# Kernel optimization log

Hardware: AMD Instinct MI355X
Metric: run time of the kernel (lower is better)

Reference implementation:

```python
import jax, jax.numpy as jnp
import numpy as np

E = 1024   # embed_size
S = 2048   # seq_len
H = 16     # heads
HD = S // H  # head_dim = 128
N = 2      # batch


def setup_inputs() -> dict:
    key = jax.random.key(0)
    ks = jax.random.split(key, 11)
    w = 0.02  # init scale to keep softmax logits well-conditioned
    return {
        "x":   jax.random.normal(ks[0], (N, E, S), dtype=jnp.float32),
        "W_r": jax.random.normal(ks[1], (S, E), dtype=jnp.float32) * w,
        "b_r": jnp.zeros((S,), dtype=jnp.float32),
        "Wq":  jax.random.normal(ks[2], (H, HD, HD), dtype=jnp.float32) * w,
        "bq":  jnp.zeros((H, HD), dtype=jnp.float32),
        "Wk":  jax.random.normal(ks[3], (H, HD, HD), dtype=jnp.float32) * w,
        "bk":  jnp.zeros((H, HD), dtype=jnp.float32),
        "Wv":  jax.random.normal(ks[4], (H, HD, HD), dtype=jnp.float32) * w,
        "bv":  jnp.zeros((H, HD), dtype=jnp.float32),
        "Wo":  jax.random.normal(ks[5], (E, S), dtype=jnp.float32) * w,
        "bo":  jnp.zeros((E,), dtype=jnp.float32),
    }


def reference(x, W_r, b_r, Wq, bq, Wk, bk, Wv, bv, Wo, bo):
    n = x.shape[0]
    # reduced[n, j, s] = sum_e W_r[j, e] * x[n, e, s] + b_r[j]
    # equals reduce_dim(x.permute(0,2,1)).permute(0,2,1): shape (N, S, S)
    reduced = jnp.einsum('je,nes->njs', W_r, x) + b_r[None, :, None]
    # split last dim into heads: (N, S, H, HD)
    r = reduced.reshape(n, S, H, HD)
    # per-head linear projections (torch Linear: y = x @ W.T + b), batched over heads
    q = jnp.einsum('nshd,hkd->hnsk', r, Wq) + bq[:, None, None, :]
    k = jnp.einsum('nshd,hkd->hnsk', r, Wk) + bk[:, None, None, :]
    v = jnp.einsum('nshd,hkd->hnsk', r, Wv) + bv[:, None, None, :]
    # attention (NO 1/sqrt(d) scaling, faithful to source)
    scores = jnp.einsum('hnqd,hnkd->hnqk', q, k)          # (H, N, S, S)
    weights = jax.nn.softmax(scores, axis=-1)
    o = jnp.einsum('hnqk,hnkd->hnqd', weights, v)          # (H, N, S, HD)
    # faithful raw reshape of the (H, N, S, HD)-contiguous tensor
    o = o.reshape(n, S, H * HD)
    return jnp.einsum('nsd,ed->nse', o, Wo) + bo           # (N, S, E)
```

## Files before the change

### kernel.cpp

```cpp
#include <hip/hip_runtime.h>

#define S_LEN 2048
#define E_DIM 1024
#define NH 16
#define HD 128
#define NB 2
#define NPAIR (NH*NB)

typedef __attribute__((ext_vector_type(4))) float f32x4;
typedef __attribute__((ext_vector_type(8))) short bf16x8;

__device__ __forceinline__ unsigned short f2bf(float f) {
    unsigned u = __builtin_bit_cast(unsigned, f);
    u += 0x7fffu + ((u >> 16) & 1u);
    return (unsigned short)(u >> 16);
}
__device__ __forceinline__ float bf2f(unsigned short h) {
    unsigned u = ((unsigned)h) << 16;
    return __builtin_bit_cast(float, u);
}
__device__ __forceinline__ unsigned cvtpk(float lo, float hi) {
    unsigned r;
    asm("v_cvt_pk_bf16_f32 %0, %1, %2" : "=v"(r) : "v"(lo), "v"(hi));
    return r;
}

__device__ __forceinline__ void gl_lds16(const unsigned short* g, unsigned short* l) {
    __builtin_amdgcn_global_load_lds((__attribute__((address_space(1))) void*)g,
                                     (__attribute__((address_space(3))) void*)l,
                                     16, 0, 0);
}

template<int OF32, int SWZ>
__global__ __launch_bounds__(256, 2) void gemm_bt(
    const unsigned short* __restrict__ A, const unsigned short* __restrict__ B,
    void* __restrict__ C,
    const float* __restrict__ brow, const float* __restrict__ bcol,
    int K, int lda, int ldb, int ldc, int zdiv,
    long long a_sh, long long a_sl, long long b_sh, long long b_sl,
    long long c_sh, long long c_sl, int brs, int bcs)
{
    __shared__ unsigned short As[2][128*64];
    __shared__ unsigned short Bs[2][128*64];
    int bm, bn, z;
    if (SWZ) {
        const int gx = gridDim.x, gy = gridDim.y;
        const int nxy = gx * gy;
        const int nwg = nxy * gridDim.z;
        const int flat = (blockIdx.z*gy + blockIdx.y)*gx + blockIdx.x;
        const int id2 = (flat & 7)*(nwg >> 3) + (flat >> 3);
        z = id2 / nxy; const int r = id2 % nxy; bm = r / gx; bn = r % gx;
    } else { bm = blockIdx.y; bn = blockIdx.x; z = blockIdx.z; }
    const int zh = z / zdiv, zl = z % zdiv;
    A += (long long)zh*a_sh + (long long)zl*a_sl;
    B += (long long)zh*b_sh + (long long)zl*b_sl;
    const long long coff = (long long)zh*c_sh + (long long)zl*c_sl;
    const int tid = threadIdx.x, wid = tid >> 6, lane = tid & 63;
    const int l3 = lane >> 3;
    const int cg = (lane & 7) ^ l3;
    const unsigned short* Ag = A + (long long)(bm*128 + wid*32 + l3)*lda + cg*8;
    const unsigned short* Bg = B + (long long)(bn*128 + wid*32 + l3)*ldb + cg*8;

    f32x4 acc[4][4];
    #pragma unroll
    for (int m = 0; m < 4; ++m)
        #pragma unroll
        for (int n = 0; n < 4; ++n)
            #pragma unroll
            for (int j = 0; j < 4; ++j) acc[m][n][j] = 0.f;

    const int r0 = lane & 15, q = lane >> 4;
    const int wr = (wid >> 1) * 64, wc = (wid & 1) * 64;

    auto stage = [&](int buf, int kt) {
        unsigned short* as = &As[buf][wid*32*64];
        unsigned short* bs = &Bs[buf][wid*32*64];
        #pragma unroll
        for (int i = 0; i < 4; ++i) {
            gl_lds16(Ag + (long long)(i*8)*lda + kt, as + i*8*64);
            gl_lds16(Bg + (long long)(i*8)*ldb + kt, bs + i*8*64);
        }
    };

    const int nt = K >> 6;
    stage(0, 0);
    __syncthreads();
    int cur = 0;
    for (int t = 0; t < nt; ++t) {
        if (t + 1 < nt) stage(cur ^ 1, (t + 1) << 6);
        #pragma unroll
        for (int ks = 0; ks < 2; ++ks) {
            bf16x8 av[4], bv[4];
            #pragma unroll
            for (int m = 0; m < 4; ++m) {
                const int ra = wr + m*16 + r0;
                av[m] = *(const bf16x8*)&As[cur][ra*64 + (((ks*4 + q) ^ (ra & 7)) << 3)];
                const int rb = wc + m*16 + r0;
                bv[m] = *(const bf16x8*)&Bs[cur][rb*64 + (((ks*4 + q) ^ (rb & 7)) << 3)];
            }
            __builtin_amdgcn_s_setprio(1);
            #pragma unroll
            for (int m = 0; m < 4; ++m)
                #pragma unroll
                for (int n = 0; n < 4; ++n)
                    acc[m][n] = __builtin_amdgcn_mfma_f32_16x16x32_bf16(
                        av[m], bv[n], acc[m][n], 0, 0, 0);
            __builtin_amdgcn_s_setprio(0);
        }
        __syncthreads();
        cur ^= 1;
    }

    const int rq = lane >> 4;
    const bool has_br = (brow != nullptr), has_bc = (bcol != nullptr);
    #pragma unroll
    for (int m = 0; m < 4; ++m) {
        #pragma unroll
        for (int n = 0; n < 4; ++n) {
            const int gcol = bn*128 + wc + n*16 + r0;
            float cb = has_bc ? bcol[(long long)bcs*zh + gcol] : 0.f;
            #pragma unroll
            for (int j = 0; j < 4; ++j) {
                const int grow = bm*128 + wr + m*16 + rq*4 + j;
                float v = acc[m][n][j] + cb;
                if (has_br) v += brow[(long long)brs*zh + grow];
                const long long idx = coff + (long long)grow*ldc + gcol;
                if (OF32) ((float*)C)[idx] = v;
                else      ((unsigned short*)C)[idx] = f2bf(v);
            }
        }
    }
}

__global__ __launch_bounds__(256, 2) void flash_attn(
    const unsigned short* __restrict__ Q,
    const unsigned short* __restrict__ Kb,
    const unsigned short* __restrict__ Vt,
    unsigned short* __restrict__ O)
{
    __shared__ unsigned short Ks[2][64*128];
    __shared__ unsigned short Vs[2][128*64];
    __shared__ unsigned short Plds[4][32*64];
    const int flat = blockIdx.y * gridDim.x + blockIdx.x;
    const int id2 = (flat & 7)*64 + (flat >> 3);
    const int pair = id2 >> 4, qt = id2 & 15;
    const int tid = threadIdx.x, wid = tid >> 6, lane = tid & 63;
    const int r0 = lane & 15, q4 = lane >> 4;
    const long long base = (long long)pair * S_LEN * HD;
    const unsigned short* Qp = Q + base + (long long)(qt*128 + wid*32) * HD;
    const unsigned short* Kp = Kb + base;
    const unsigned short* Vp = Vt + base;
    unsigned short* P = &Plds[wid][0];

    const int krow = wid*16 + (lane >> 4);
    const int kc0  = (lane & 15) ^ (lane >> 4);
    const int vrow = wid*32 + (lane >> 3);
    const int vc0  = (lane & 7) ^ (lane >> 3);

    auto stageK = [&](int buf, int kv) {
        #pragma unroll
        for (int i = 0; i < 4; ++i)
            gl_lds16(Kp + (long long)(kv + krow + i*4)*HD + ((kc0 ^ ((i & 1) << 2))*8),
                     &Ks[buf][(wid*16 + i*4)*128]);
    };
    auto stageV = [&](int buf, int kv) {
        #pragma unroll
        for (int i = 0; i < 4; ++i)
            gl_lds16(Vp + (long long)(vrow + i*8)*S_LEN + kv + vc0*8,
                     &Vs[buf][(wid*32 + i*8)*64]);
    };

    bf16x8 qfr[2][4];
    #pragma unroll
    for (int qf = 0; qf < 2; ++qf)
        #pragma unroll
        for (int ks = 0; ks < 4; ++ks)
            qfr[qf][ks] = *(const bf16x8*)&Qp[(qf*16 + r0)*HD + ks*32 + q4*8];

    f32x4 o_acc[2][8];
    #pragma unroll
    for (int qf = 0; qf < 2; ++qf)
        #pragma unroll
        for (int nf = 0; nf < 8; ++nf)
            #pragma unroll
            for (int j = 0; j < 4; ++j) o_acc[qf][nf][j] = 0.f;
    float m_[2] = {-3.0e38f, -3.0e38f}, l_[2] = {0.f, 0.f};

    stageK(0, 0); stageV(0, 0);
    __syncthreads();
    int cur = 0;
    for (int kv = 0; kv < S_LEN; kv += 64) {
        if (kv + 64 < S_LEN) { stageK(cur ^ 1, kv + 64); stageV(cur ^ 1, kv + 64); }
        f32x4 sacc[4][2];
        #pragma unroll
        for (int kf = 0; kf < 4; ++kf)
            #pragma unroll
            for (int qf = 0; qf < 2; ++qf)
                #pragma unroll
                for (int j = 0; j < 4; ++j) sacc[kf][qf][j] = 0.f;
        #pragma unroll
        for (int ks = 0; ks < 4; ++ks) {
            bf16x8 kfr[4];
            #pragma unroll
            for (int kf = 0; kf < 4; ++kf) {
                const int row = kf*16 + r0;
                kfr[kf] = *(const bf16x8*)&Ks[cur][row*128 + (((ks*4 + q4) ^ (r0 & 7)) << 3)];
            }
            __builtin_amdgcn_s_setprio(1);
            #pragma unroll
            for (int kf = 0; kf < 4; ++kf)
                #pragma unroll
                for (int qf = 0; qf < 2; ++qf)
                    sacc[kf][qf] = __builtin_amdgcn_mfma_f32_16x16x32_bf16(
                        kfr[kf], qfr[qf][ks], sacc[kf][qf], 0, 0, 0);
            __builtin_amdgcn_s_setprio(0);
        }
        #pragma unroll
        for (int qf = 0; qf < 2; ++qf) {
            float t0 = fmaxf(fmaxf(sacc[0][qf][0], sacc[0][qf][1]),
                             fmaxf(sacc[0][qf][2], sacc[0][qf][3]));
            float t1 = fmaxf(fmaxf(sacc[1][qf][0], sacc[1][qf][1]),
                             fmaxf(sacc[1][qf][2], sacc[1][qf][3]));
            float t2 = fmaxf(fmaxf(sacc[2][qf][0], sacc[2][qf][1]),
                             fmaxf(sacc[2][qf][2], sacc[2][qf][3]));
            float t3 = fmaxf(fmaxf(sacc[3][qf][0], sacc[3][qf][1]),
                             fmaxf(sacc[3][qf][2], sacc[3][qf][3]));
            float tmax = fmaxf(fmaxf(t0, t1), fmaxf(t2, t3));
            tmax = fmaxf(tmax, __shfl_xor(tmax, 16));
            tmax = fmaxf(tmax, __shfl_xor(tmax, 32));
            if (__all(tmax <= m_[qf] + 8.f)) {
                float tsum = 0.f;
                #pragma unroll
                for (int kf = 0; kf < 4; ++kf)
                    #pragma unroll
                    for (int j = 0; j < 4; ++j) {
                        const float e = __expf(sacc[kf][qf][j] - m_[qf]);
                        sacc[kf][qf][j] = e; tsum += e;
                    }
                tsum += __shfl_xor(tsum, 16);
                tsum += __shfl_xor(tsum, 32);
                l_[qf] += tsum;
            } else {
                const float mnew = fmaxf(m_[qf], tmax);
                const float scale = __expf(m_[qf] - mnew);
                float tsum = 0.f;
                #pragma unroll
                for (int kf = 0; kf < 4; ++kf)
                    #pragma unroll
                    for (int j = 0; j < 4; ++j) {
                        const float e = __expf(sacc[kf][qf][j] - mnew);
                        sacc[kf][qf][j] = e; tsum += e;
                    }
                tsum += __shfl_xor(tsum, 16);
                tsum += __shfl_xor(tsum, 32);
                l_[qf] = l_[qf]*scale + tsum;
                m_[qf] = mnew;
                float sc[4];
                #pragma unroll
                for (int j = 0; j < 4; ++j) sc[j] = __shfl(scale, (q4*4 + j) | (lane & 48));
                #pragma unroll
                for (int nf = 0; nf < 8; ++nf)
                    #pragma unroll
                    for (int j = 0; j < 4; ++j) o_acc[qf][nf][j] *= sc[j];
            }
        }
        #pragma unroll
        for (int qf = 0; qf < 2; ++qf)
            #pragma unroll
            for (int kf = 0; kf < 4; ++kf) {
                uint2 pk;
                pk.x = cvtpk(sacc[kf][qf][0], sacc[kf][qf][1]);
                pk.y = cvtpk(sacc[kf][qf][2], sacc[kf][qf][3]);
                const int row = qf*16 + r0;
                const int byte = (row*128 + kf*32 + q4*8) ^ ((row & 7) << 4);
                *(uint2*)((char*)P + byte) = pk;
            }
        #pragma unroll
        for (int c = 0; c < 2; ++c) {
            bf16x8 pa[2];
            #pragma unroll
            for (int qf = 0; qf < 2; ++qf) {
                const int row = qf*16 + r0;
                const int byte = (row*128 + c*64 + q4*16) ^ ((row & 7) << 4);
                pa[qf] = *(const bf16x8*)((char*)P + byte);
            }
            bf16x8 vb[8];
            #pragma unroll
            for (int nf = 0; nf < 8; ++nf) {
                const int row = nf*16 + r0;
                vb[nf] = *(const bf16x8*)&Vs[cur][row*64 + (((c*4 + q4) ^ (r0 & 7)) << 3)];
            }
            __builtin_amdgcn_s_setprio(1);
            #pragma unroll
            for (int nf = 0; nf < 8; ++nf)
                #pragma unroll
                for (int qf = 0; qf < 2; ++qf)
                    o_acc[qf][nf] = __builtin_amdgcn_mfma_f32_16x16x32_bf16(
                        pa[qf], vb[nf], o_acc[qf][nf], 0, 0, 0);
            __builtin_amdgcn_s_setprio(0);
        }
        __syncthreads();
        cur ^= 1;
    }
    #pragma unroll
    for (int qf = 0; qf < 2; ++qf) {
        const float inv = 1.f / l_[qf];
        float iv[4];
        #pragma unroll
        for (int j = 0; j < 4; ++j) iv[j] = __shfl(inv, (q4*4 + j) | (lane & 48));
        #pragma unroll
        for (int nf = 0; nf < 8; ++nf)
            #pragma unroll
            for (int j = 0; j < 4; ++j) {
                const int grow = qt*128 + wid*32 + qf*16 + q4*4 + j;
                O[base + (long long)grow*HD + nf*16 + r0] = f2bf(o_acc[qf][nf][j] * iv[j]);
            }
    }
}

__global__ __launch_bounds__(256) void transpose_conv(
    const float* __restrict__ x, unsigned short* __restrict__ xT)
{
    __shared__ float t[32][33];
    const int n = blockIdx.z;
    const int e0 = blockIdx.y * 32, s0 = blockIdx.x * 32;
    const int tx = threadIdx.x & 31, ty = threadIdx.x >> 5;
    #pragma unroll
    for (int i = 0; i < 4; ++i) {
        const int e = ty + i*8;
        t[e][tx] = x[((long long)n*E_DIM + e0 + e)*S_LEN + s0 + tx];
    }
    __syncthreads();
    #pragma unroll
    for (int i = 0; i < 4; ++i) {
        const int s = ty + i*8;
        xT[((long long)n*S_LEN + s0 + s)*E_DIM + e0 + tx] = f2bf(t[tx][s]);
    }
}

__global__ __launch_bounds__(256) void conv_bf16(
    const float* __restrict__ in, unsigned short* __restrict__ out, int n8)
{
    const int i = blockIdx.x * 256 + threadIdx.x;
    if (i >= n8) return;
    const float4 a = ((const float4*)in)[2*i];
    const float4 b = ((const float4*)in)[2*i + 1];
    unsigned short u[8] = {f2bf(a.x), f2bf(a.y), f2bf(a.z), f2bf(a.w),
                           f2bf(b.x), f2bf(b.y), f2bf(b.z), f2bf(b.w)};
    ((uint4*)out)[i] = *(const uint4*)u;
}

extern "C" void kernel_launch(void* const* d_in, const int* in_sizes, int n_in,
                              void* d_out, int out_size, void* d_ws, size_t ws_size,
                              hipStream_t stream)
{
    const float* x   = (const float*)d_in[0];
    const float* W_r = (const float*)d_in[1];
    const float* b_r = (const float*)d_in[2];
    const float* Wq  = (const float*)d_in[3];
    const float* bq  = (const float*)d_in[4];
    const float* Wk  = (const float*)d_in[5];
    const float* bk  = (const float*)d_in[6];
    const float* Wv  = (const float*)d_in[7];
    const float* bv  = (const float*)d_in[8];
    const float* Wo  = (const float*)d_in[9];
    const float* bo  = (const float*)d_in[10];
    float* out = (float*)d_out;
    (void)in_sizes; (void)n_in; (void)out_size; (void)ws_size;

    char* w = (char*)d_ws;
    size_t off = 0;
    auto take = [&](size_t bytes) -> unsigned short* {
        unsigned short* p = (unsigned short*)(w + off);
        off = (off + bytes + 255) & ~(size_t)255;
        return p;
    };
    unsigned short* Wr_b = take((size_t)S_LEN*E_DIM*2);
    unsigned short* xT_b = take((size_t)NB*S_LEN*E_DIM*2);
    unsigned short* Wq_b = take((size_t)NH*HD*HD*2);
    unsigned short* Wk_b = take((size_t)NH*HD*HD*2);
    unsigned short* Wv_b = take((size_t)NH*HD*HD*2);
    unsigned short* Wo_b = take((size_t)E_DIM*S_LEN*2);
    unsigned short* Rd_b = take((size_t)NB*S_LEN*S_LEN*2);
    unsigned short* Q_b  = take((size_t)NPAIR*S_LEN*HD*2);
    unsigned short* K_b  = take((size_t)NPAIR*S_LEN*HD*2);
    unsigned short* Vt_b = take((size_t)NPAIR*HD*S_LEN*2);
    unsigned short* O_b  = take((size_t)NPAIR*S_LEN*HD*2);

    conv_bf16<<<dim3((S_LEN*E_DIM/8 + 255)/256), 256, 0, stream>>>(W_r, Wr_b, S_LEN*E_DIM/8);
    conv_bf16<<<dim3((NH*HD*HD/8 + 255)/256), 256, 0, stream>>>(Wq, Wq_b, NH*HD*HD/8);
    conv_bf16<<<dim3((NH*HD*HD/8 + 255)/256), 256, 0, stream>>>(Wk, Wk_b, NH*HD*HD/8);
    conv_bf16<<<dim3((NH*HD*HD/8 + 255)/256), 256, 0, stream>>>(Wv, Wv_b, NH*HD*HD/8);
    conv_bf16<<<dim3((E_DIM*S_LEN/8 + 255)/256), 256, 0, stream>>>(Wo, Wo_b, E_DIM*S_LEN/8);
    transpose_conv<<<dim3(S_LEN/32, E_DIM/32, NB), 256, 0, stream>>>(x, xT_b);

    gemm_bt<0,1><<<dim3(S_LEN/128, S_LEN/128, NB), 256, 0, stream>>>(
        Wr_b, xT_b, Rd_b, b_r, nullptr,
        E_DIM, E_DIM, E_DIM, S_LEN, 1,
        0LL, 0LL, (long long)S_LEN*E_DIM, 0LL, (long long)S_LEN*S_LEN, 0LL, 0, 0);

    gemm_bt<0,1><<<dim3(HD/128, S_LEN/128, NPAIR), 256, 0, stream>>>(
        Rd_b, Wq_b, Q_b, nullptr, bq,
        HD, S_LEN, HD, HD, NB,
        128LL, (long long)S_LEN*S_LEN, (long long)HD*HD, 0LL,
        (long long)NB*S_LEN*HD, (long long)S_LEN*HD, 0, HD);
    gemm_bt<0,1><<<dim3(HD/128, S_LEN/128, NPAIR), 256, 0, stream>>>(
        Rd_b, Wk_b, K_b, nullptr, bk,
        HD, S_LEN, HD, HD, NB,
        128LL, (long long)S_LEN*S_LEN, (long long)HD*HD, 0LL,
        (long long)NB*S_LEN*HD, (long long)S_LEN*HD, 0, HD);
    gemm_bt<0,1><<<dim3(S_LEN/128, HD/128, NPAIR), 256, 0, stream>>>(
        Wv_b, Rd_b, Vt_b, bv, nullptr,
        HD, HD, S_LEN, S_LEN, NB,
        (long long)HD*HD, 0LL, 128LL, (long long)S_LEN*S_LEN,
        (long long)NB*HD*S_LEN, (long long)HD*S_LEN, HD, 0);

    flash_attn<<<dim3(S_LEN/128, NPAIR), 256, 0, stream>>>(Q_b, K_b, Vt_b, O_b);

    gemm_bt<1,1><<<dim3(E_DIM/128, S_LEN/128, NB), 256, 0, stream>>>(
        O_b, Wo_b, out, nullptr, bo,
        S_LEN, S_LEN, S_LEN, E_DIM, 1,
        (long long)S_LEN*S_LEN, 0LL, 0LL, 0LL, (long long)S_LEN*E_DIM, 0LL, 0, 0);
}
```

Before: 302.3 us.

## Fuse Q/K/V projections into one GEMM and shrink flash-attention KV tile

Stacks Wq, Wk and Wv per head into one weight matrix with a packing kernel, and computes all three projections in a single qkv_gemm launch. Q and K are written interleaved into one buffer and V is written transposed. This replaces three projection GEMMs and three weight-conversion launches, and reads the reduced activation once instead of three times. Flash attention now uses a 32-wide KV tile with smaller LDS buffers and launch bounds raised to 4 blocks per SM for occupancy, at the cost of twice as many loop iterations and barriers. The transposed V store in qkv_gemm is strided and may coalesce poorly.

```diff
diff --git a/kernel.cpp b/kernel.cpp
--- a/kernel.cpp
+++ b/kernel.cpp
@@ -14,10 +14,6 @@
     unsigned u = __builtin_bit_cast(unsigned, f);
     u += 0x7fffu + ((u >> 16) & 1u);
     return (unsigned short)(u >> 16);
-}
-__device__ __forceinline__ float bf2f(unsigned short h) {
-    unsigned u = ((unsigned)h) << 16;
-    return __builtin_bit_cast(float, u);
 }
 __device__ __forceinline__ unsigned cvtpk(float lo, float hi) {
     unsigned r;
@@ -132,42 +128,142 @@
     }
 }
 
-__global__ __launch_bounds__(256, 2) void flash_attn(
-    const unsigned short* __restrict__ Q,
-    const unsigned short* __restrict__ Kb,
+__global__ __launch_bounds__(256, 2) void qkv_gemm(
+    const unsigned short* __restrict__ Rd,
+    const unsigned short* __restrict__ Wstk,
+    const float* __restrict__ bstk,
+    unsigned short* __restrict__ QK,
+    unsigned short* __restrict__ Vt)
+{
+    __shared__ unsigned short As[2][128*64];
+    __shared__ unsigned short Bs[2][128*64];
+    const int gx = gridDim.x, gy = gridDim.y;
+    const int nxy = gx * gy;
+    const int nwg = nxy * gridDim.z;
+    const int flat = (blockIdx.z*gy + blockIdx.y)*gx + blockIdx.x;
+    const int id2 = (flat & 7)*(nwg >> 3) + (flat >> 3);
+    const int z = id2 / nxy; const int r = id2 % nxy;
+    const int bm = r / gx, bn = r % gx;
+    const int h = z >> 1, nb = z & 1;
+    const unsigned short* A = Rd + (long long)nb*S_LEN*S_LEN + h*128;
+    const unsigned short* B = Wstk + (long long)h*384*128 + (long long)bn*128*128;
+    const int tid = threadIdx.x, wid = tid >> 6, lane = tid & 63;
+    const int l3 = lane >> 3;
+    const int cg = (lane & 7) ^ l3;
+    const unsigned short* Ag = A + (long long)(bm*128 + wid*32 + l3)*S_LEN + cg*8;
+    const unsigned short* Bg = B + (long long)(wid*32 + l3)*HD + cg*8;
+
+    f32x4 acc[4][4];
+    #pragma unroll
+    for (int m = 0; m < 4; ++m)
+        #pragma unroll
+        for (int n = 0; n < 4; ++n)
+            #pragma unroll
+            for (int j = 0; j < 4; ++j) acc[m][n][j] = 0.f;
+
+    const int r0 = lane & 15, q = lane >> 4;
+    const int wr = (wid >> 1) * 64, wc = (wid & 1) * 64;
+
+    auto stage = [&](int buf, int kt) {
+        unsigned short* as = &As[buf][wid*32*64];
+        unsigned short* bs = &Bs[buf][wid*32*64];
+        #pragma unroll
+        for (int i = 0; i < 4; ++i) {
+            gl_lds16(Ag + (long long)(i*8)*S_LEN + kt, as + i*8*64);
+            gl_lds16(Bg + (long long)(i*8)*HD + kt, bs + i*8*64);
+        }
+    };
+
+    stage(0, 0);
+    __syncthreads();
+    int cur = 0;
+    #pragma unroll
+    for (int t = 0; t < 2; ++t) {
+        if (t == 0) stage(1, 64);
+        #pragma unroll
+        for (int ks = 0; ks < 2; ++ks) {
+            bf16x8 av[4], bv[4];
+            #pragma unroll
+            for (int m = 0; m < 4; ++m) {
+                const int ra = wr + m*16 + r0;
+                av[m] = *(const bf16x8*)&As[cur][ra*64 + (((ks*4 + q) ^ (ra & 7)) << 3)];
+                const int rb = wc + m*16 + r0;
+                bv[m] = *(const bf16x8*)&Bs[cur][rb*64 + (((ks*4 + q) ^ (rb & 7)) << 3)];
+            }
+            __builtin_amdgcn_s_setprio(1);
+            #pragma unroll
+            for (int m = 0; m < 4; ++m)
+                #pragma unroll
+                for (int n = 0; n < 4; ++n)
+                    acc[m][n] = __builtin_amdgcn_mfma_f32_16x16x32_bf16(
+                        av[m], bv[n], acc[m][n], 0, 0, 0);
+            __builtin_amdgcn_s_setprio(0);
+        }
+        __syncthreads();
+        cur ^= 1;
+    }
+
+    const int rq = lane >> 4;
+    #pragma unroll
+    for (int m = 0; m < 4; ++m) {
+        #pragma unroll
+        for (int n = 0; n < 4; ++n) {
+            const int lcol = wc + n*16 + r0;
+            const float cb = bstk[h*384 + bn*128 + lcol];
+            #pragma unroll
+            for (int j = 0; j < 4; ++j) {
+                const int grow = bm*128 + wr + m*16 + rq*4 + j;
+                const float v = acc[m][n][j] + cb;
+                if (bn < 2)
+                    QK[(long long)z*S_LEN*256 + (long long)grow*256 + bn*128 + lcol] = f2bf(v);
+                else
+                    Vt[(long long)z*HD*S_LEN + (long long)lcol*S_LEN + grow] = f2bf(v);
+            }
+        }
+    }
+}
+
+__global__ __launch_bounds__(256, 4) void flash_attn(
+    const unsigned short* __restrict__ QK,
     const unsigned short* __restrict__ Vt,
     unsigned short* __restrict__ O)
 {
-    __shared__ unsigned short Ks[2][64*128];
-    __shared__ unsigned short Vs[2][128*64];
-    __shared__ unsigned short Plds[4][32*64];
+    __shared__ unsigned short Ks[2][32*128];
+    __shared__ unsigned short Vs[2][128*32];
+    __shared__ unsigned short Plds[4][32*32];
     const int flat = blockIdx.y * gridDim.x + blockIdx.x;
     const int id2 = (flat & 7)*64 + (flat >> 3);
     const int pair = id2 >> 4, qt = id2 & 15;
     const int tid = threadIdx.x, wid = tid >> 6, lane = tid & 63;
     const int r0 = lane & 15, q4 = lane >> 4;
-    const long long base = (long long)pair * S_LEN * HD;
-    const unsigned short* Qp = Q + base + (long long)(qt*128 + wid*32) * HD;
-    const unsigned short* Kp = Kb + base;
-    const unsigned short* Vp = Vt + base;
+    const long long qkbase = (long long)pair * S_LEN * 256;
+    const unsigned short* Qp = QK + qkbase + (long long)(qt*128 + wid*32) * 256;
+    const unsigned short* Kp = QK + qkbase + 128;
+    const unsigned short* Vp = Vt + (long long)pair * HD * S_LEN;
     unsigned short* P = &Plds[wid][0];
 
-    const int krow = wid*16 + (lane >> 4);
-    const int kc0  = (lane & 15) ^ (lane >> 4);
-    const int vrow = wid*32 + (lane >> 3);
-    const int vc0  = (lane & 7) ^ (lane >> 3);
+    const int kr_l = lane >> 4;
+    const int kc_l = lane & 15;
+    const int vr_l = lane >> 2;
+    const int vc_l = lane & 3;
 
     auto stageK = [&](int buf, int kv) {
         #pragma unroll
-        for (int i = 0; i < 4; ++i)
-            gl_lds16(Kp + (long long)(kv + krow + i*4)*HD + ((kc0 ^ ((i & 1) << 2))*8),
-                     &Ks[buf][(wid*16 + i*4)*128]);
+        for (int i = 0; i < 2; ++i) {
+            const int srow = wid*8 + i*4 + kr_l;
+            const int sc = kc_l ^ (srow & 7);
+            gl_lds16(Kp + (long long)(kv + srow)*256 + sc*8,
+                     &Ks[buf][(wid*8 + i*4)*128]);
+        }
     };
     auto stageV = [&](int buf, int kv) {
         #pragma unroll
-        for (int i = 0; i < 4; ++i)
-            gl_lds16(Vp + (long long)(vrow + i*8)*S_LEN + kv + vc0*8,
-                     &Vs[buf][(wid*32 + i*8)*64]);
+        for (int i = 0; i < 2; ++i) {
+            const int srow = wid*32 + i*16 + vr_l;
+            const int sc = vc_l ^ (srow & 3);
+            gl_lds16(Vp + (long long)srow*S_LEN + kv + sc*8,
+                     &Vs[buf][(wid*32 + i*16)*32]);
+        }
     };
 
     bf16x8 qfr[2][4];
@@ -175,7 +271,7 @@
     for (int qf = 0; qf < 2; ++qf)
         #pragma unroll
         for (int ks = 0; ks < 4; ++ks)
-            qfr[qf][ks] = *(const bf16x8*)&Qp[(qf*16 + r0)*HD + ks*32 + q4*8];
+            qfr[qf][ks] = *(const bf16x8*)&Qp[(qf*16 + r0)*256 + ks*32 + q4*8];
 
     f32x4 o_acc[2][8];
     #pragma unroll
@@ -189,26 +285,26 @@
     stageK(0, 0); stageV(0, 0);
     __syncthreads();
     int cur = 0;
-    for (int kv = 0; kv < S_LEN; kv += 64) {
-        if (kv + 64 < S_LEN) { stageK(cur ^ 1, kv + 64); stageV(cur ^ 1, kv + 64); }
-        f32x4 sacc[4][2];
-        #pragma unroll
-        for (int kf = 0; kf < 4; ++kf)
+    for (int kv = 0; kv < S_LEN; kv += 32) {
+        if (kv + 32 < S_LEN) { stageK(cur ^ 1, kv + 32); stageV(cur ^ 1, kv + 32); }
+        f32x4 sacc[2][2];
+        #pragma unroll
+        for (int kf = 0; kf < 2; ++kf)
             #pragma unroll
             for (int qf = 0; qf < 2; ++qf)
                 #pragma unroll
                 for (int j = 0; j < 4; ++j) sacc[kf][qf][j] = 0.f;
         #pragma unroll
         for (int ks = 0; ks < 4; ++ks) {
-            bf16x8 kfr[4];
-            #pragma unroll
-            for (int kf = 0; kf < 4; ++kf) {
+            bf16x8 kfr[2];
+            #pragma unroll
+            for (int kf = 0; kf < 2; ++kf) {
                 const int row = kf*16 + r0;
                 kfr[kf] = *(const bf16x8*)&Ks[cur][row*128 + (((ks*4 + q4) ^ (r0 & 7)) << 3)];
             }
             __builtin_amdgcn_s_setprio(1);
             #pragma unroll
-            for (int kf = 0; kf < 4; ++kf)
+            for (int kf = 0; kf < 2; ++kf)
                 #pragma unroll
                 for (int qf = 0; qf < 2; ++qf)
                     sacc[kf][qf] = __builtin_amdgcn_mfma_f32_16x16x32_bf16(
@@ -221,17 +317,13 @@
                              fmaxf(sacc[0][qf][2], sacc[0][qf][3]));
             float t1 = fmaxf(fmaxf(sacc[1][qf][0], sacc[1][qf][1]),
                              fmaxf(sacc[1][qf][2], sacc[1][qf][3]));
-            float t2 = fmaxf(fmaxf(sacc[2][qf][0], sacc[2][qf][1]),
-                             fmaxf(sacc[2][qf][2], sacc[2][qf][3]));
-            float t3 = fmaxf(fmaxf(sacc[3][qf][0], sacc[3][qf][1]),
-                             fmaxf(sacc[3][qf][2], sacc[3][qf][3]));
-            float tmax = fmaxf(fmaxf(t0, t1), fmaxf(t2, t3));
+            float tmax = fmaxf(t0, t1);
             tmax = fmaxf(tmax, __shfl_xor(tmax, 16));
             tmax = fmaxf(tmax, __shfl_xor(tmax, 32));
             if (__all(tmax <= m_[qf] + 8.f)) {
                 float tsum = 0.f;
                 #pragma unroll
-                for (int kf = 0; kf < 4; ++kf)
+                for (int kf = 0; kf < 2; ++kf)
                     #pragma unroll
                     for (int j = 0; j < 4; ++j) {
                         const float e = __expf(sacc[kf][qf][j] - m_[qf]);
@@ -245,7 +337,7 @@
                 const float scale = __expf(m_[qf] - mnew);
                 float tsum = 0.f;
                 #pragma unroll
-                for (int kf = 0; kf < 4; ++kf)
+                for (int kf = 0; kf < 2; ++kf)
                     #pragma unroll
                     for (int j = 0; j < 4; ++j) {
                         const float e = __expf(sacc[kf][qf][j] - mnew);
@@ -267,28 +359,27 @@
         #pragma unroll
         for (int qf = 0; qf < 2; ++qf)
             #pragma unroll
-            for (int kf = 0; kf < 4; ++kf) {
+            for (int kf = 0; kf < 2; ++kf) {
                 uint2 pk;
                 pk.x = cvtpk(sacc[kf][qf][0], sacc[kf][qf][1]);
                 pk.y = cvtpk(sacc[kf][qf][2], sacc[kf][qf][3]);
                 const int row = qf*16 + r0;
-                const int byte = (row*128 + kf*32 + q4*8) ^ ((row & 7) << 4);
+                const int byte = row*64 + ((kf*32 + q4*8) ^ ((row & 3) << 4));
                 *(uint2*)((char*)P + byte) = pk;
             }
-        #pragma unroll
-        for (int c = 0; c < 2; ++c) {
+        {
             bf16x8 pa[2];
             #pragma unroll
             for (int qf = 0; qf < 2; ++qf) {
                 const int row = qf*16 + r0;
-                const int byte = (row*128 + c*64 + q4*16) ^ ((row & 7) << 4);
+                const int byte = row*64 + ((q4*16) ^ ((row & 3) << 4));
                 pa[qf] = *(const bf16x8*)((char*)P + byte);
             }
             bf16x8 vb[8];
             #pragma unroll
             for (int nf = 0; nf < 8; ++nf) {
                 const int row = nf*16 + r0;
-                vb[nf] = *(const bf16x8*)&Vs[cur][row*64 + (((c*4 + q4) ^ (r0 & 7)) << 3)];
+                vb[nf] = *(const bf16x8*)&Vs[cur][row*32 + ((q4 ^ (r0 & 3)) << 3)];
             }
             __builtin_amdgcn_s_setprio(1);
             #pragma unroll
@@ -302,6 +393,7 @@
         __syncthreads();
         cur ^= 1;
     }
+    const long long obase = (long long)pair * S_LEN * HD;
     #pragma unroll
     for (int qf = 0; qf < 2; ++qf) {
         const float inv = 1.f / l_[qf];
@@ -313,7 +405,7 @@
             #pragma unroll
             for (int j = 0; j < 4; ++j) {
                 const int grow = qt*128 + wid*32 + qf*16 + q4*4 + j;
-                O[base + (long long)grow*HD + nf*16 + r0] = f2bf(o_acc[qf][nf][j] * iv[j]);
+                O[obase + (long long)grow*HD + nf*16 + r0] = f2bf(o_acc[qf][nf][j] * iv[j]);
             }
     }
 }
@@ -348,6 +440,32 @@
     unsigned short u[8] = {f2bf(a.x), f2bf(a.y), f2bf(a.z), f2bf(a.w),
                            f2bf(b.x), f2bf(b.y), f2bf(b.z), f2bf(b.w)};
     ((uint4*)out)[i] = *(const uint4*)u;
+}
+
+__global__ __launch_bounds__(256) void qkv_pack(
+    const float* __restrict__ Wq, const float* __restrict__ Wk,
+    const float* __restrict__ Wv, const float* __restrict__ bq,
+    const float* __restrict__ bk, const float* __restrict__ bv,
+    unsigned short* __restrict__ Wstk, float* __restrict__ bstk)
+{
+    const int i8 = blockIdx.x*256 + threadIdx.x;
+    const int per_h = 384*16;
+    const int h = i8 / per_h, rem = i8 - h*per_h;
+    const int rr = rem >> 4, c8 = rem & 15;
+    const int rl = rr & 127;
+    const float* src = (rr < 128) ? Wq : (rr < 256) ? Wk : Wv;
+    const float* p = src + ((long long)h*128 + rl)*128 + c8*8;
+    const float4 a = ((const float4*)p)[0];
+    const float4 b = ((const float4*)p)[1];
+    unsigned short u[8] = {f2bf(a.x), f2bf(a.y), f2bf(a.z), f2bf(a.w),
+                           f2bf(b.x), f2bf(b.y), f2bf(b.z), f2bf(b.w)};
+    ((uint4*)Wstk)[i8] = *(const uint4*)u;
+    if (i8 < NH*384) {
+        const int h2 = i8 / 384, r2 = i8 - h2*384;
+        bstk[i8] = (r2 < 128) ? bq[h2*128 + r2]
+                 : (r2 < 256) ? bk[h2*128 + r2 - 128]
+                              : bv[h2*128 + r2 - 256];
+    }
 }
 
 extern "C" void kernel_launch(void* const* d_in, const int* in_sizes, int n_in,
@@ -375,47 +493,29 @@
         off = (off + bytes + 255) & ~(size_t)255;
         return p;
     };
-    unsigned short* Wr_b = take((size_t)S_LEN*E_DIM*2);
-    unsigned short* xT_b = take((size_t)NB*S_LEN*E_DIM*2);
-    unsigned short* Wq_b = take((size_t)NH*HD*HD*2);
-    unsigned short* Wk_b = take((size_t)NH*HD*HD*2);
-    unsigned short* Wv_b = take((size_t)NH*HD*HD*2);
-    unsigned short* Wo_b = take((size_t)E_DIM*S_LEN*2);
-    unsigned short* Rd_b = take((size_t)NB*S_LEN*S_LEN*2);
-    unsigned short* Q_b  = take((size_t)NPAIR*S_LEN*HD*2);
-    unsigned short* K_b  = take((size_t)NPAIR*S_LEN*HD*2);
-    unsigned short* Vt_b = take((size_t)NPAIR*HD*S_LEN*2);
-    unsigned short* O_b  = take((size_t)NPAIR*S_LEN*HD*2);
+    unsigned short* Wr_b  = take((size_t)S_LEN*E_DIM*2);
+    unsigned short* xT_b  = take((size_t)NB*S_LEN*E_DIM*2);
+    unsigned short* Wstk  = take((size_t)NH*384*HD*2);
+    float*          bstk  = (float*)take((size_t)NH*384*4);
+    unsigned short* Wo_b  = take((size_t)E_DIM*S_LEN*2);
+    unsigned short* Rd_b  = take((size_t)NB*S_LEN*S_LEN*2);
+    unsigned short* QK_b  = take((size_t)NPAIR*S_LEN*256*2);
+    unsigned short* Vt_b  = take((size_t)NPAIR*HD*S_LEN*2);
+    unsigned short* O_b   = take((size_t)NPAIR*S_LEN*HD*2);
 
     conv_bf16<<<dim3((S_LEN*E_DIM/8 + 255)/256), 256, 0, stream>>>(W_r, Wr_b, S_LEN*E_DIM/8);
-    conv_bf16<<<dim3((NH*HD*HD/8 + 255)/256), 256, 0, stream>>>(Wq, Wq_b, NH*HD*HD/8);
-    conv_bf16<<<dim3((NH*HD*HD/8 + 255)/256), 256, 0, stream>>>(Wk, Wk_b, NH*HD*HD/8);
-    conv_bf16<<<dim3((NH*HD*HD/8 + 255)/256), 256, 0, stream>>>(Wv, Wv_b, NH*HD*HD/8);
     conv_bf16<<<dim3((E_DIM*S_LEN/8 + 255)/256), 256, 0, stream>>>(Wo, Wo_b, E_DIM*S_LEN/8);
     transpose_conv<<<dim3(S_LEN/32, E_DIM/32, NB), 256, 0, stream>>>(x, xT_b);
+    qkv_pack<<<dim3(NH*384*16/256), 256, 0, stream>>>(Wq, Wk, Wv, bq, bk, bv, Wstk, bstk);
 
     gemm_bt<0,1><<<dim3(S_LEN/128, S_LEN/128, NB), 256, 0, stream>>>(
         Wr_b, xT_b, Rd_b, b_r, nullptr,
         E_DIM, E_DIM, E_DIM, S_LEN, 1,
         0LL, 0LL, (long long)S_LEN*E_DIM, 0LL, (long long)S_LEN*S_LEN, 0LL, 0, 0);
 
-    gemm_bt<0,1><<<dim3(HD/128, S_LEN/128, NPAIR), 256, 0, stream>>>(
-        Rd_b, Wq_b, Q_b, nullptr, bq,
-        HD, S_LEN, HD, HD, NB,
-        128LL, (long long)S_LEN*S_LEN, (long long)HD*HD, 0LL,
-        (long long)NB*S_LEN*HD, (long long)S_LEN*HD, 0, HD);
-    gemm_bt<0,1><<<dim3(HD/128, S_LEN/128, NPAIR), 256, 0, stream>>>(
-        Rd_b, Wk_b, K_b, nullptr, bk,
-        HD, S_LEN, HD, HD, NB,
-        128LL, (long long)S_LEN*S_LEN, (long long)HD*HD, 0LL,
-        (long long)NB*S_LEN*HD, (long long)S_LEN*HD, 0, HD);
-    gemm_bt<0,1><<<dim3(S_LEN/128, HD/128, NPAIR), 256, 0, stream>>>(
-        Wv_b, Rd_b, Vt_b, bv, nullptr,
-        HD, HD, S_LEN, S_LEN, NB,
-        (long long)HD*HD, 0LL, 128LL, (long long)S_LEN*S_LEN,
-        (long long)NB*HD*S_LEN, (long long)HD*S_LEN, HD, 0);
-
-    flash_attn<<<dim3(S_LEN/128, NPAIR), 256, 0, stream>>>(Q_b, K_b, Vt_b, O_b);
+    qkv_gemm<<<dim3(3, S_LEN/128, NPAIR), 256, 0, stream>>>(Rd_b, Wstk, bstk, QK_b, Vt_b);
+
+    flash_attn<<<dim3(S_LEN/128, NPAIR), 256, 0, stream>>>(QK_b, Vt_b, O_b);
 
     gemm_bt<1,1><<<dim3(E_DIM/128, S_LEN/128, NB), 256, 0, stream>>>(
         O_b, Wo_b, out, nullptr, bo,
```

Result: slower. 836.7 us (+176.7%).
